# Optimization experiments

Hardware: AMD Instinct MI355X
Metric: run time of the kernel (lower is better)

The kernel has to match this reference:

```python
import jax, jax.numpy as jnp
import numpy as np

D_MODEL = 1024
N_HEADS = 16
HEAD_DIM = D_MODEL // N_HEADS
NEG_INF = jnp.float32(-1e30)


def setup_inputs() -> dict:
    key = jax.random.key(0)
    ks = jax.random.split(key, 5)
    B, S, D = 4, 2048, D_MODEL
    scale = 1.0 / np.sqrt(D)
    x = jax.random.normal(ks[0], (B, S, D), dtype=jnp.float32)
    # packed in-projection like torch nn.MultiheadAttention: [3D, D] weight, [3D] bias
    w_qkv = jax.random.normal(ks[1], (3 * D, D), dtype=jnp.float32) * scale
    b_qkv = jnp.zeros((3 * D,), dtype=jnp.float32)
    w_out = jax.random.normal(ks[2], (D, D), dtype=jnp.float32) * scale
    b_out = jnp.zeros((D,), dtype=jnp.float32)
    return {"x": x, "w_qkv": w_qkv, "b_qkv": b_qkv, "w_out": w_out, "b_out": b_out}


def _alibi_causal_mask(S, dtype):
    # mask[q, k] = -(q - k) if k <= q else -inf  (causal + ALiBi distance bias)
    q = jnp.arange(S)[:, None]
    k = jnp.arange(S)[None, :]
    return jnp.where(k <= q, -(q - k).astype(dtype), NEG_INF)


def reference(x, w_qkv, b_qkv, w_out, b_out):
    B, S, D = x.shape
    H, hd = N_HEADS, HEAD_DIM
    qkv = x @ w_qkv.T + b_qkv                      # [B, S, 3D]
    q, k, v = jnp.split(qkv, 3, axis=-1)
    # [B, H, S, hd]
    q = q.reshape(B, S, H, hd).transpose(0, 2, 1, 3)
    k = k.reshape(B, S, H, hd).transpose(0, 2, 1, 3)
    v = v.reshape(B, S, H, hd).transpose(0, 2, 1, 3)
    scores = jnp.einsum('bhqd,bhkd->bhqk', q, k) / np.sqrt(hd)
    scores = scores + _alibi_causal_mask(S, scores.dtype)  # same bias all heads
    probs = jax.nn.softmax(scores, axis=-1)        # dropout inactive at eval
    out = jnp.einsum('bhqk,bhkd->bhqd', probs, v)  # [B, H, S, hd]
    out = out.transpose(0, 2, 1, 3).reshape(B, S, D)
    return out @ w_out.T + b_out
```

## Files before the change

### kernel.cpp

```cpp
#include <hip/hip_runtime.h>


typedef __bf16 bf16;
typedef __bf16 bf16x8 __attribute__((ext_vector_type(8)));
typedef float  f32x4  __attribute__((ext_vector_type(4)));
typedef float  f32x16 __attribute__((ext_vector_type(16)));

#define NEGINF2 (-3.0e38f)
#define LOG2E 1.4426950408889634f
#define QKSCALE 0.18033688011112042f

__device__ __forceinline__ void gll16(const void* g, void* l) {
  __builtin_amdgcn_global_load_lds(
      (const __attribute__((address_space(1))) void*)g,
      (__attribute__((address_space(3))) void*)l, 16, 0, 0);
}

__global__ __launch_bounds__(256) void cvt_bf16(const float* __restrict__ in,
                                                bf16* __restrict__ out, int n8) {
  int i = blockIdx.x * 256 + threadIdx.x;
  if (i >= n8) return;
  const float4* p = (const float4*)in;
  float4 a = p[2 * i], b = p[2 * i + 1];
  bf16x8 r;
  r[0] = (bf16)a.x; r[1] = (bf16)a.y; r[2] = (bf16)a.z; r[3] = (bf16)a.w;
  r[4] = (bf16)b.x; r[5] = (bf16)b.y; r[6] = (bf16)b.z; r[7] = (bf16)b.w;
  *(bf16x8*)(out + 8 * i) = r;
}

template <int OUTF32>
__global__ __launch_bounds__(256) void gemm_bt(const bf16* __restrict__ A,
                                               const bf16* __restrict__ Bt,
                                               const float* __restrict__ bias,
                                               void* __restrict__ Cout,
                                               int M, int N, int K) {
  __shared__ bf16 As[128 * 32];
  __shared__ bf16 Bs[128 * 32];
  const int tid = threadIdx.x;
  const int w = tid >> 6, l = tid & 63;
  const int t = l & 15, g = l >> 4;
  const int wr = w >> 1, wc = w & 1;
  const int tiles_n = N >> 7;
  const int bm = blockIdx.x / tiles_n, bn = blockIdx.x % tiles_n;
  const bf16* Ab = A + (long)(bm * 128) * K;
  const bf16* Bb = Bt + (long)(bn * 128) * K;

  f32x4 acc[4][4] = {};

  const int srow = w * 16 + (l >> 2);
  const int scol = (l & 3) * 8;
  char* AsB = (char*)As;
  char* BsB = (char*)Bs;

  for (int kt = 0; kt < K; kt += 32) {
    __syncthreads();
    gll16(Ab + (long)(srow)*K + kt + scol,      AsB + w * 1024);
    gll16(Ab + (long)(srow + 64) * K + kt + scol, AsB + 4096 + w * 1024);
    gll16(Bb + (long)(srow)*K + kt + scol,      BsB + w * 1024);
    gll16(Bb + (long)(srow + 64) * K + kt + scol, BsB + 4096 + w * 1024);
    __syncthreads();

    bf16x8 af[4], bfr[4];
#pragma unroll
    for (int m = 0; m < 4; m++)
      af[m] = *(const bf16x8*)(AsB + (wr * 64 + m * 16 + t) * 64 + g * 16);
#pragma unroll
    for (int n = 0; n < 4; n++)
      bfr[n] = *(const bf16x8*)(BsB + (wc * 64 + n * 16 + t) * 64 + g * 16);
#pragma unroll
    for (int m = 0; m < 4; m++)
#pragma unroll
      for (int n = 0; n < 4; n++)
        acc[m][n] = __builtin_amdgcn_mfma_f32_16x16x32_bf16(af[m], bfr[n], acc[m][n], 0, 0, 0);
  }

#pragma unroll
  for (int m = 0; m < 4; m++) {
#pragma unroll
    for (int n = 0; n < 4; n++) {
      const int col = bn * 128 + wc * 64 + n * 16 + t;
      const float bv = bias[wc * 64 + n * 16 + t + bn * 128];
#pragma unroll
      for (int r = 0; r < 4; r++) {
        const int row = bm * 128 + wr * 64 + m * 16 + 4 * g + r;
        const float v = acc[m][n][r] + bv;
        if (OUTF32)
          ((float*)Cout)[(long)row * N + col] = v;
        else
          ((bf16*)Cout)[(long)row * N + col] = (bf16)v;
      }
    }
  }
}

__global__ __launch_bounds__(256) void transpose_v(const bf16* __restrict__ qkv,
                                                   bf16* __restrict__ vT) {
  __shared__ bf16 tile[64][72];
  const int bid = blockIdx.x;
  const int st = bid & 31, bh = bid >> 5;
  const int b = bh >> 4, h = bh & 15;
  const int tid = threadIdx.x;
  const int r = tid >> 3, c = tid & 7;

#pragma unroll
  for (int i = 0; i < 2; i++) {
    const int row = r + i * 32;
    const bf16* src =
        qkv + ((long)(b * 2048 + st * 64 + row)) * 3072 + 2048 + h * 64 + c * 8;
    bf16x8 v = *(const bf16x8*)src;
#pragma unroll
    for (int j = 0; j < 8; j++) tile[row][c * 8 + j] = v[j];
  }
  __syncthreads();
#pragma unroll
  for (int i = 0; i < 2; i++) {
    const int d = r + i * 32;
    bf16x8 o;
#pragma unroll
    for (int j = 0; j < 8; j++) o[j] = tile[c * 8 + j][d];
    *(bf16x8*)(vT + ((long)bh * 64 + d) * 2048 + st * 64 + c * 8) = o;
  }
}

__device__ __forceinline__ unsigned pk2(float a, float b) {
  union { bf16 h[2]; unsigned u; } t;
  t.h[0] = (bf16)a; t.h[1] = (bf16)b;
  return t.u;
}

__global__ __launch_bounds__(256) void attn_fwd4(const bf16* __restrict__ qkv,
                                                 const bf16* __restrict__ vT,
                                                 bf16* __restrict__ outp) {
  __shared__ bf16 Ks[2][64 * 64];
  __shared__ bf16 Vs[2][64 * 64];
  const int bid = blockIdx.x;
  const int pair = bid >> 6;
  const int bh = bid & 63;
  const int b = bh >> 4, h = bh & 15;
  const int tid = threadIdx.x;
  const int w = tid >> 6, l = tid & 63;
  const int ql = l & 31, hi = l >> 5;
  const long tokbase = (long)b * 2048;

  const bf16* Kg = qkv + tokbase * 3072 + 1024 + h * 64;
  const bf16* Vg = vT + (long)bh * 64 * 2048;
  const int r8 = l >> 3, c8 = l & 7;
  const int swc = c8 ^ r8;
  const int rx = ql & 7;

#define STAGE(c, kv)                                                          \
  {                                                                           \
    _Pragma("unroll") for (int i = 0; i < 2; i++) {                           \
      gll16(Kg + (long)((kv) + i * 32 + w * 8 + r8) * 3072 + swc * 8,         \
            (char*)Ks + (c)*8192 + i * 4096 + w * 1024);                      \
      gll16(Vg + (long)(i * 32 + w * 8 + r8) * 2048 + (kv) + swc * 8,         \
            (char*)Vs + (c)*8192 + i * 4096 + w * 1024);                      \
    }                                                                         \
  }

  for (int pass = 0; pass < 2; ++pass) {
    const int qt = pass ? pair : (15 - pair);
    const int q0w = qt * 128 + w * 32;
    const int qg = q0w + ql;
    const int qmax = q0w + 31;

    bf16x8 qf[4];
    {
      const bf16* qp = qkv + (tokbase + qg) * 3072 + h * 64 + hi * 8;
#pragma unroll
      for (int kk = 0; kk < 4; kk++) qf[kk] = *(const bf16x8*)(qp + kk * 16);
    }

    f32x16 o0, o1;
#pragma unroll
    for (int r = 0; r < 16; r++) { o0[r] = 0.f; o1[r] = 0.f; }
    float m2 = NEGINF2, lsum = 0.f;

    const int kvend = qt * 128 + 128;
    STAGE(0, 0);

    for (int kv0 = 0; kv0 < kvend; kv0 += 64) {
      const int cur = (kv0 >> 6) & 1;
      const bool pre = (kv0 + 64 < kvend);
      if (pre) STAGE(cur ^ 1, kv0 + 64);
      if (pre) asm volatile("s_waitcnt vmcnt(4)" ::: "memory");
      else     asm volatile("s_waitcnt vmcnt(0)" ::: "memory");
      __builtin_amdgcn_s_barrier();
      asm volatile("" ::: "memory");

      if (kv0 <= qmax) {
        const int nt = (kv0 + 32 <= qmax) ? 2 : 1;
        const char* Kb = (const char*)Ks + cur * 8192;
        const char* Vb = (const char*)Vs + cur * 8192;

        float sc[2][16];
#pragma unroll
        for (int tt = 0; tt < 2; tt++) {
          if (tt < nt) {
            bf16x8 kf[4];
#pragma unroll
            for (int kk = 0; kk < 4; kk++)
              kf[kk] = *(const bf16x8*)(Kb + (tt * 32 + ql) * 128 +
                                        (((kk << 1) + hi) ^ rx) * 16);
            f32x16 s;
#pragma unroll
            for (int r = 0; r < 16; r++) s[r] = 0.f;
#pragma unroll
            for (int kk = 0; kk < 4; kk++)
              s = __builtin_amdgcn_mfma_f32_32x32x16_bf16(kf[kk], qf[kk], s, 0, 0, 0);

            const int dbase = kv0 + tt * 32 + 4 * hi - qg;
            const float fb = (float)dbase * LOG2E;
            const bool full = (kv0 + tt * 32 + 31) <= q0w;
            if (full) {
#pragma unroll
              for (int r = 0; r < 16; r++) {
                const float cr = (float)((r & 3) + 8 * (r >> 2)) * LOG2E;
                sc[tt][r] = fmaf(s[r], QKSCALE, fb) + cr;
              }
            } else {
#pragma unroll
              for (int r = 0; r < 16; r++) {
                const int cri = (r & 3) + 8 * (r >> 2);
                const float cr = (float)cri * LOG2E;
                const float v = fmaf(s[r], QKSCALE, fb) + cr;
                sc[tt][r] = (dbase + cri > 0) ? NEGINF2 : v;
              }
            }
          }
        }

        bf16x8 vf0[4], vf1[4];
#pragma unroll
        for (int c = 0; c < 4; c++) {
          if (c < 2 * nt) {
            const int cd = (((c << 1) + hi) ^ rx) * 16;
            vf0[c] = *(const bf16x8*)(Vb + ql * 128 + cd);
            vf1[c] = *(const bf16x8*)(Vb + (32 + ql) * 128 + cd);
          }
        }

        float mp0 = NEGINF2, mp1 = NEGINF2, mp2 = NEGINF2, mp3 = NEGINF2;
#pragma unroll
        for (int tt = 0; tt < 2; tt++) {
          if (tt < nt) {
            mp0 = fmaxf(mp0, fmaxf(sc[tt][0], sc[tt][4]));
            mp1 = fmaxf(mp1, fmaxf(sc[tt][1], sc[tt][5]));
            mp2 = fmaxf(mp2, fmaxf(sc[tt][2], sc[tt][6]));
            mp3 = fmaxf(mp3, fmaxf(sc[tt][3], sc[tt][7]));
            mp0 = fmaxf(mp0, fmaxf(sc[tt][8], sc[tt][12]));
            mp1 = fmaxf(mp1, fmaxf(sc[tt][9], sc[tt][13]));
            mp2 = fmaxf(mp2, fmaxf(sc[tt][10], sc[tt][14]));
            mp3 = fmaxf(mp3, fmaxf(sc[tt][11], sc[tt][15]));
          }
        }
        float mx = fmaxf(fmaxf(mp0, mp1), fmaxf(mp2, mp3));
        mx = fmaxf(mx, __shfl_xor(mx, 32, 64));
        mx = fmaxf(mx, m2);
        const float alpha = exp2f(m2 - mx);
        m2 = mx;

        float rs0 = 0.f, rs1 = 0.f, rs2 = 0.f, rs3 = 0.f;
#pragma unroll
        for (int tt = 0; tt < 2; tt++) {
          if (tt < nt) {
#pragma unroll
            for (int r = 0; r < 16; r++) {
              const float p = exp2f(sc[tt][r] - mx);
              sc[tt][r] = p;
              if ((r & 3) == 0) rs0 += p; else if ((r & 3) == 1) rs1 += p;
              else if ((r & 3) == 2) rs2 += p; else rs3 += p;
            }
          }
        }
        float rs = (rs0 + rs1) + (rs2 + rs3);
        rs += __shfl_xor(rs, 32, 64);
        lsum = lsum * alpha + rs;
        o0 *= alpha;
        o1 *= alpha;

        bf16x8 pf[4];
#pragma unroll
        for (int tt = 0; tt < 2; tt++) {
          if (tt < nt) {
            unsigned W0 = pk2(sc[tt][0], sc[tt][1]),  W1 = pk2(sc[tt][2], sc[tt][3]);
            unsigned W2 = pk2(sc[tt][4], sc[tt][5]),  W3 = pk2(sc[tt][6], sc[tt][7]);
            unsigned W4 = pk2(sc[tt][8], sc[tt][9]),  W5 = pk2(sc[tt][10], sc[tt][11]);
            unsigned W6 = pk2(sc[tt][12], sc[tt][13]), W7 = pk2(sc[tt][14], sc[tt][15]);
            const unsigned X0 = __shfl_xor(hi ? W0 : W2, 32, 64);
            const unsigned X1 = __shfl_xor(hi ? W1 : W3, 32, 64);
            const unsigned X2 = __shfl_xor(hi ? W4 : W6, 32, 64);
            const unsigned X3 = __shfl_xor(hi ? W5 : W7, 32, 64);
            union { unsigned u[4]; bf16x8 v; } f0, f1;
            f0.u[0] = hi ? X0 : W0;  f0.u[1] = hi ? X1 : W1;
            f0.u[2] = hi ? W2 : X0;  f0.u[3] = hi ? W3 : X1;
            f1.u[0] = hi ? X2 : W4;  f1.u[1] = hi ? X3 : W5;
            f1.u[2] = hi ? W6 : X2;  f1.u[3] = hi ? W7 : X3;
            pf[tt * 2 + 0] = f0.v;
            pf[tt * 2 + 1] = f1.v;
          }
        }

#pragma unroll
        for (int c = 0; c < 4; c++) {
          if (c < 2 * nt) {
            o0 = __builtin_amdgcn_mfma_f32_32x32x16_bf16(vf0[c], pf[c], o0, 0, 0, 0);
            o1 = __builtin_amdgcn_mfma_f32_32x32x16_bf16(vf1[c], pf[c], o1, 0, 0, 0);
          }
        }
      }

      asm volatile("" ::: "memory");
      __builtin_amdgcn_s_barrier();
    }

    const float inv = 1.f / lsum;
    bf16* orow = outp + (tokbase + qg) * 1024 + h * 64 + 4 * hi;
#pragma unroll
    for (int rq = 0; rq < 4; rq++) {
      union { bf16 h[4]; unsigned u[2]; } p0, p1;
#pragma unroll
      for (int j = 0; j < 4; j++) {
        p0.h[j] = (bf16)(o0[rq * 4 + j] * inv);
        p1.h[j] = (bf16)(o1[rq * 4 + j] * inv);
      }
      *(unsigned*)(orow + rq * 8) = p0.u[0];
      *(unsigned*)(orow + rq * 8 + 2) = p0.u[1];
      *(unsigned*)(orow + 32 + rq * 8) = p1.u[0];
      *(unsigned*)(orow + 32 + rq * 8 + 2) = p1.u[1];
    }
  }
#undef STAGE
}

extern "C" void kernel_launch(void* const* d_in, const int* in_sizes, int n_in,
                              void* d_out, int out_size, void* d_ws, size_t ws_size,
                              hipStream_t stream) {
  (void)in_sizes; (void)n_in; (void)out_size; (void)ws_size;
  const float* x     = (const float*)d_in[0];
  const float* w_qkv = (const float*)d_in[1];
  const float* b_qkv = (const float*)d_in[2];
  const float* w_out = (const float*)d_in[3];
  const float* b_out = (const float*)d_in[4];
  float* out = (float*)d_out;

  char* ws = (char*)d_ws;
  bf16* xb    = (bf16*)(ws);
  bf16* wqkvb = (bf16*)(ws + 16777216);
  bf16* woutb = (bf16*)(ws + 23068672);
  bf16* qkvb  = (bf16*)(ws + 25165824);
  bf16* vTb   = (bf16*)(ws + 75497472);
  bf16* attb  = xb;

  cvt_bf16<<<4096, 256, 0, stream>>>(x, xb, 8192 * 1024 / 8);
  cvt_bf16<<<1536, 256, 0, stream>>>(w_qkv, wqkvb, 3072 * 1024 / 8);
  cvt_bf16<<<512, 256, 0, stream>>>(w_out, woutb, 1024 * 1024 / 8);

  gemm_bt<0><<<64 * 24, 256, 0, stream>>>(xb, wqkvb, b_qkv, (void*)qkvb, 8192, 3072, 1024);
  transpose_v<<<2048, 256, 0, stream>>>(qkvb, vTb);
  attn_fwd4<<<512, 256, 0, stream>>>(qkvb, vTb, attb);
  gemm_bt<1><<<64 * 8, 256, 0, stream>>>(attb, woutb, b_out, (void*)out, 8192, 1024, 1024);
}
```

Baseline: 311.1 us.

## Double-buffer GEMM LDS loads and iterate attention KV backwards with lazy rescale

The GEMM now double-buffers its A/B tiles in LDS, prefetching the next K-slice via global_load_lds while MFMAs run on the current one. This replaces the two full barriers per iteration with a waitcnt plus barrier. Attention walks KV blocks from the diagonal backwards, so the running max is established early. It then skips the output rescale whenever the new block max stays within a threshold of the current max. This removes most exp2 and rescale work, at the cost of extra LDS in the GEMM and a bounded growth of unnormalized values.

```diff
diff --git a/kernel.cpp b/kernel.cpp
--- a/kernel.cpp
+++ b/kernel.cpp
@@ -9,6 +9,7 @@
 #define NEGINF2 (-3.0e38f)
 #define LOG2E 1.4426950408889634f
 #define QKSCALE 0.18033688011112042f
+#define DEFER_THR 8.0f
 
 __device__ __forceinline__ void gll16(const void* g, void* l) {
   __builtin_amdgcn_global_load_lds(
@@ -34,8 +35,8 @@
                                                const float* __restrict__ bias,
                                                void* __restrict__ Cout,
                                                int M, int N, int K) {
-  __shared__ bf16 As[128 * 32];
-  __shared__ bf16 Bs[128 * 32];
+  __shared__ bf16 As[2][128 * 32];
+  __shared__ bf16 Bs[2][128 * 32];
   const int tid = threadIdx.x;
   const int w = tid >> 6, l = tid & 63;
   const int t = l & 15, g = l >> 4;
@@ -49,17 +50,31 @@
 
   const int srow = w * 16 + (l >> 2);
   const int scol = (l & 3) * 8;
-  char* AsB = (char*)As;
-  char* BsB = (char*)Bs;
-
+
+#define GSTAGE(c, kt)                                                          \
+  {                                                                            \
+    gll16(Ab + (long)(srow)*K + (kt) + scol,                                   \
+          (char*)As + (c)*8192 + w * 1024);                                    \
+    gll16(Ab + (long)(srow + 64) * K + (kt) + scol,                            \
+          (char*)As + (c)*8192 + 4096 + w * 1024);                             \
+    gll16(Bb + (long)(srow)*K + (kt) + scol,                                   \
+          (char*)Bs + (c)*8192 + w * 1024);                                    \
+    gll16(Bb + (long)(srow + 64) * K + (kt) + scol,                            \
+          (char*)Bs + (c)*8192 + 4096 + w * 1024);                             \
+  }
+
+  GSTAGE(0, 0);
   for (int kt = 0; kt < K; kt += 32) {
-    __syncthreads();
-    gll16(Ab + (long)(srow)*K + kt + scol,      AsB + w * 1024);
-    gll16(Ab + (long)(srow + 64) * K + kt + scol, AsB + 4096 + w * 1024);
-    gll16(Bb + (long)(srow)*K + kt + scol,      BsB + w * 1024);
-    gll16(Bb + (long)(srow + 64) * K + kt + scol, BsB + 4096 + w * 1024);
-    __syncthreads();
-
+    const int cur = (kt >> 5) & 1;
+    const bool pre = (kt + 32 < K);
+    if (pre) GSTAGE(cur ^ 1, kt + 32);
+    if (pre) asm volatile("s_waitcnt vmcnt(4)" ::: "memory");
+    else     asm volatile("s_waitcnt vmcnt(0)" ::: "memory");
+    __builtin_amdgcn_s_barrier();
+    asm volatile("" ::: "memory");
+
+    const char* AsB = (const char*)As + cur * 8192;
+    const char* BsB = (const char*)Bs + cur * 8192;
     bf16x8 af[4], bfr[4];
 #pragma unroll
     for (int m = 0; m < 4; m++)
@@ -72,7 +87,11 @@
 #pragma unroll
       for (int n = 0; n < 4; n++)
         acc[m][n] = __builtin_amdgcn_mfma_f32_16x16x32_bf16(af[m], bfr[n], acc[m][n], 0, 0, 0);
-  }
+
+    asm volatile("" ::: "memory");
+    __builtin_amdgcn_s_barrier();
+  }
+#undef GSTAGE
 
 #pragma unroll
   for (int m = 0; m < 4; m++) {
@@ -128,7 +147,7 @@
   return t.u;
 }
 
-__global__ __launch_bounds__(256) void attn_fwd4(const bf16* __restrict__ qkv,
+__global__ __launch_bounds__(256) void attn_fwd5(const bf16* __restrict__ qkv,
                                                  const bf16* __restrict__ vT,
                                                  bf16* __restrict__ outp) {
   __shared__ bf16 Ks[2][64 * 64];
@@ -177,12 +196,13 @@
     float m2 = NEGINF2, lsum = 0.f;
 
     const int kvend = qt * 128 + 128;
-    STAGE(0, 0);
-
-    for (int kv0 = 0; kv0 < kvend; kv0 += 64) {
-      const int cur = (kv0 >> 6) & 1;
-      const bool pre = (kv0 + 64 < kvend);
-      if (pre) STAGE(cur ^ 1, kv0 + 64);
+    STAGE(0, kvend - 64);
+
+    int it = 0;
+    for (int kv0 = kvend - 64; kv0 >= 0; kv0 -= 64, ++it) {
+      const int cur = it & 1;
+      const bool pre = (kv0 > 0);
+      if (pre) STAGE(cur ^ 1, kv0 - 64);
       if (pre) asm volatile("s_waitcnt vmcnt(4)" ::: "memory");
       else     asm volatile("s_waitcnt vmcnt(0)" ::: "memory");
       __builtin_amdgcn_s_barrier();
@@ -254,11 +274,16 @@
             mp3 = fmaxf(mp3, fmaxf(sc[tt][11], sc[tt][15]));
           }
         }
-        float mx = fmaxf(fmaxf(mp0, mp1), fmaxf(mp2, mp3));
-        mx = fmaxf(mx, __shfl_xor(mx, 32, 64));
-        mx = fmaxf(mx, m2);
-        const float alpha = exp2f(m2 - mx);
-        m2 = mx;
+        float pmax = fmaxf(fmaxf(mp0, mp1), fmaxf(mp2, mp3));
+        pmax = fmaxf(pmax, __shfl_xor(pmax, 32, 64));
+        if (!__all(pmax <= m2 + DEFER_THR)) {
+          const float mx = fmaxf(pmax, m2);
+          const float alpha = exp2f(m2 - mx);
+          m2 = mx;
+          lsum *= alpha;
+          o0 *= alpha;
+          o1 *= alpha;
+        }
 
         float rs0 = 0.f, rs1 = 0.f, rs2 = 0.f, rs3 = 0.f;
 #pragma unroll
@@ -266,7 +291,7 @@
           if (tt < nt) {
 #pragma unroll
             for (int r = 0; r < 16; r++) {
-              const float p = exp2f(sc[tt][r] - mx);
+              const float p = exp2f(sc[tt][r] - m2);
               sc[tt][r] = p;
               if ((r & 3) == 0) rs0 += p; else if ((r & 3) == 1) rs1 += p;
               else if ((r & 3) == 2) rs2 += p; else rs3 += p;
@@ -275,9 +300,7 @@
         }
         float rs = (rs0 + rs1) + (rs2 + rs3);
         rs += __shfl_xor(rs, 32, 64);
-        lsum = lsum * alpha + rs;
-        o0 *= alpha;
-        o1 *= alpha;
+        lsum += rs;
 
         bf16x8 pf[4];
 #pragma unroll
@@ -358,6 +381,6 @@
 
   gemm_bt<0><<<64 * 24, 256, 0, stream>>>(xb, wqkvb, b_qkv, (void*)qkvb, 8192, 3072, 1024);
   transpose_v<<<2048, 256, 0, stream>>>(qkvb, vTb);
-  attn_fwd4<<<512, 256, 0, stream>>>(qkvb, vTb, attb);
+  attn_fwd5<<<512, 256, 0, stream>>>(qkvb, vTb, attb);
   gemm_bt<1><<<64 * 8, 256, 0, stream>>>(attb, woutb, b_out, (void*)out, 8192, 1024, 1024);
 }
```

After: 349.4 us. +12.3%, slower.
